# Performance work log

Measured on AMD Instinct MI355X. Metric: run time of the kernel, lower is better.

The kernel has to match this reference:

```python
import jax, jax.numpy as jnp
import numpy as np

HEADS = 4
DIM_HEAD = 32


def setup_inputs() -> dict:
    key = jax.random.key(0)
    k1, k2, k3, k4 = jax.random.split(key, 4)
    dim = 64
    hidden = HEADS * DIM_HEAD  # 128
    x = jax.random.normal(k1, (1, dim, 16, 16, 16), jnp.float32)
    # Conv3d 1x1 kernels collapse to [out_ch, in_ch] matrices
    w_qkv = jax.random.normal(k2, (hidden * 3, dim), jnp.float32) * 0.05
    w_out = jax.random.normal(k3, (dim, hidden), jnp.float32) * 0.05
    b_out = jax.random.normal(k4, (dim,), jnp.float32) * 0.05
    return {"x": x, "w_qkv": w_qkv, "w_out": w_out, "b_out": b_out}


def reference(x, w_qkv, w_out, b_out):
    scale = DIM_HEAD ** -0.5
    b, c, dz, dy, dx = x.shape
    n = dz * dy * dx
    xf = x.reshape(b, c, n)  # flatten spatial dims
    # 1x1 Conv3d (no bias) == channel matmul: [b, 3*hidden, n]
    qkv = jnp.einsum('oc,bcn->bon', w_qkv, xf)
    q, k, v = jnp.split(qkv, 3, axis=1)  # each [b, hidden, n]
    def split_heads(t):
        return t.reshape(b, HEADS, DIM_HEAD, n)  # [b, h, d, n]
    q, k, v = split_heads(q), split_heads(k), split_heads(v)
    q = q * scale
    # sim[b,h,i,j] = sum_d q[b,h,d,i] k[b,h,d,j]
    sim = jnp.einsum('bhdi,bhdj->bhij', q, k)
    sim = sim - jax.lax.stop_gradient(jnp.max(sim, axis=-1, keepdims=True))
    attn = jax.nn.softmax(sim, axis=-1)
    # out[b,h,i,d] = sum_j attn[b,h,i,j] v[b,h,d,j]
    out = jnp.einsum('bhij,bhdj->bhid', attn, v)
    # 'b h (z y x) d -> b (h d) z y x'
    out = out.transpose(0, 1, 3, 2).reshape(b, HEADS * DIM_HEAD, n)
    # final 1x1 Conv3d with bias
    y = jnp.einsum('oc,bcn->bon', w_out, out) + b_out[None, :, None]
    return y.reshape(b, -1, dz, dy, dx)
```

## Files before the change

kernel.cpp:

```cpp
#include <hip/hip_runtime.h>


typedef _Float16 f16x8 __attribute__((ext_vector_type(8)));
typedef _Float16 f16x4 __attribute__((ext_vector_type(4)));
typedef _Float16 f16x2v __attribute__((ext_vector_type(2)));
typedef __fp16 fp16x2n __attribute__((ext_vector_type(2)));
typedef float f32x4 __attribute__((ext_vector_type(4)));

static __device__ inline f16x4 pack4(float a, float b, float c, float d) {
  f16x4 r;
  r.x = (_Float16)a; r.y = (_Float16)b; r.z = (_Float16)c; r.w = (_Float16)d;
  return r;
}
static __device__ inline f16x4 pack4_rtz(float a, float b, float c, float d) {
  fp16x2n lo = __builtin_amdgcn_cvt_pkrtz(a, b);
  fp16x2n hi = __builtin_amdgcn_cvt_pkrtz(c, d);
  f16x4 r;
  r.x = (_Float16)lo.x; r.y = (_Float16)lo.y;
  r.z = (_Float16)hi.x; r.w = (_Float16)hi.y;
  return r;
}
static __device__ inline f16x2v pack2(float a, float b) {
  f16x2v r;
  r.x = (_Float16)a; r.y = (_Float16)b;
  return r;
}

__global__ __launch_bounds__(256) void qkv_kernel(
    const float* __restrict__ x, const float* __restrict__ w,
    _Float16* __restrict__ qo, _Float16* __restrict__ ko, _Float16* __restrict__ vo)
{
  __shared__ __align__(16) float xs[64 * 68];
  __shared__ __align__(16) float wsb[32 * 68];
  const int t = threadIdx.x;
  const int n0 = blockIdx.x * 64;
  const int o0 = blockIdx.y * 32;
  #pragma unroll
  for (int i = 0; i < 4; ++i) {
    int ch = t + i * 256;
    int c = ch >> 4, p = ch & 15;
    *reinterpret_cast<float4*>(&xs[c * 68 + p * 4]) =
        *reinterpret_cast<const float4*>(&x[c * 4096 + n0 + p * 4]);
  }
  #pragma unroll
  for (int i = 0; i < 2; ++i) {
    int ch = t + i * 256;
    int o = ch >> 4, p = ch & 15;
    *reinterpret_cast<float4*>(&wsb[o * 68 + p * 4]) =
        *reinterpret_cast<const float4*>(&w[(o0 + o) * 64 + p * 4]);
  }
  __syncthreads();
  const int oL = (t >> 5) * 4;
  const int nL = (t & 31) * 2;
  float acc[4][2] = {};
  for (int c4 = 0; c4 < 64; c4 += 4) {
    float2 xa[4];
    #pragma unroll
    for (int k = 0; k < 4; ++k)
      xa[k] = *reinterpret_cast<const float2*>(&xs[(c4 + k) * 68 + nL]);
    #pragma unroll
    for (int i = 0; i < 4; ++i) {
      float4 wv = *reinterpret_cast<const float4*>(&wsb[(oL + i) * 68 + c4]);
      acc[i][0] += wv.x * xa[0].x + wv.y * xa[1].x + wv.z * xa[2].x + wv.w * xa[3].x;
      acc[i][1] += wv.x * xa[0].y + wv.y * xa[1].y + wv.z * xa[2].y + wv.w * xa[3].y;
    }
  }
  const float qs = 0.17677669529663689f * 1.4426950408889634f;
  if (o0 < 128) {
    int ho = o0 >> 5;
    #pragma unroll
    for (int j = 0; j < 2; ++j) {
      int n = n0 + nL + j;
      *reinterpret_cast<f16x4*>(&qo[(ho * 4096 + n) * 32 + oL]) =
          pack4(acc[0][j] * qs, acc[1][j] * qs, acc[2][j] * qs, acc[3][j] * qs);
    }
  } else if (o0 < 256) {
    int ho = (o0 - 128) >> 5;
    #pragma unroll
    for (int j = 0; j < 2; ++j) {
      int n = n0 + nL + j;
      *reinterpret_cast<f16x4*>(&ko[(ho * 4096 + n) * 32 + oL]) =
          pack4(acc[0][j], acc[1][j], acc[2][j], acc[3][j]);
    }
  } else {
    #pragma unroll
    for (int i = 0; i < 4; ++i) {
      *reinterpret_cast<f16x2v*>(&vo[(size_t)(o0 - 256 + oL + i) * 4096 + n0 + nL]) =
          pack2(acc[i][0], acc[i][1]);
    }
  }
}

__global__ __launch_bounds__(512, 4) void attn_kernel(
    const _Float16* __restrict__ qg, const _Float16* __restrict__ kg,
    const _Float16* __restrict__ vg, _Float16* __restrict__ Opart,
    float* __restrict__ lpart, int jlen)
{
  __shared__ __align__(16) _Float16 Ks[2][64 * 40];
  __shared__ __align__(16) _Float16 Vs[2][32 * 72];
  const int t = threadIdx.x;
  const int ck = blockIdx.x;
  const int qt = blockIdx.y;
  const int h  = blockIdx.z;
  const int w = t >> 6;
  const int lane = t & 63;
  const int m = lane & 15;
  const int quad = lane >> 4;
  const int qw = qt * 256 + w * 32;

  f16x8 aq[2];
  #pragma unroll
  for (int g = 0; g < 2; ++g)
    aq[g] = *reinterpret_cast<const f16x8*>(
        &qg[(h * 4096 + qw + g * 16 + m) * 32 + quad * 8]);

  f32x4 acc[2][2];
  #pragma unroll
  for (int g = 0; g < 2; ++g) {
    acc[g][0] = f32x4{0.f, 0.f, 0.f, 0.f};
    acc[g][1] = f32x4{0.f, 0.f, 0.f, 0.f};
  }
  float ls[2] = {0.f, 0.f};

  const int jbeg = ck * jlen;
  const bool isK = (t < 256);
  const _Float16* gp;
  int ldsoff;
  if (isK) {
    int kr = t >> 2, ksg = t & 3;
    gp = kg + (size_t)(h * 4096 + jbeg + kr) * 32 + ksg * 8;
    ldsoff = kr * 40 + ksg * 8;
  } else {
    int c = t - 256, vr = c >> 3, vsg = c & 7;
    gp = vg + (size_t)(h * 32 + vr) * 4096 + jbeg + vsg * 8;
    ldsoff = vr * 72 + vsg * 8;
  }

  if (isK)
    *reinterpret_cast<uint4*>(&Ks[0][ldsoff]) = *reinterpret_cast<const uint4*>(gp);
  else
    *reinterpret_cast<uint4*>(&Vs[0][ldsoff]) = *reinterpret_cast<const uint4*>(gp);
  __syncthreads();

  for (int it = 0; it < jlen; it += 64) {
    const int buf = (it >> 6) & 1;
    if (it + 64 < jlen) {
      if (isK)
        *reinterpret_cast<uint4*>(&Ks[buf ^ 1][ldsoff]) =
            *reinterpret_cast<const uint4*>(gp + (size_t)(it + 64) * 32);
      else
        *reinterpret_cast<uint4*>(&Vs[buf ^ 1][ldsoff]) =
            *reinterpret_cast<const uint4*>(gp + (it + 64));
    }
    #pragma unroll
    for (int jt = 0; jt < 4; ++jt) {
      f16x8 kf = *reinterpret_cast<const f16x8*>(&Ks[buf][(jt * 16 + m) * 40 + quad * 8]);
      f16x4 vf0 = *reinterpret_cast<const f16x4*>(&Vs[buf][m * 72 + jt * 16 + quad * 4]);
      f16x4 vf1 = *reinterpret_cast<const f16x4*>(&Vs[buf][(16 + m) * 72 + jt * 16 + quad * 4]);
      f32x4 z = {0.f, 0.f, 0.f, 0.f};
      f32x4 sT[2];
      #pragma unroll
      for (int g = 0; g < 2; ++g)
        sT[g] = __builtin_amdgcn_mfma_f32_16x16x32_f16(kf, aq[g], z, 0, 0, 0);
      #pragma unroll
      for (int g = 0; g < 2; ++g) {
        float p0 = exp2f(sT[g][0]), p1 = exp2f(sT[g][1]);
        float p2 = exp2f(sT[g][2]), p3 = exp2f(sT[g][3]);
        ls[g] += (p0 + p1) + (p2 + p3);
        f16x4 p = pack4_rtz(p0, p1, p2, p3);
        acc[g][0] = __builtin_amdgcn_mfma_f32_16x16x16f16(p, vf0, acc[g][0], 0, 0, 0);
        acc[g][1] = __builtin_amdgcn_mfma_f32_16x16x16f16(p, vf1, acc[g][1], 0, 0, 0);
      }
    }
    __syncthreads();
  }

  #pragma unroll
  for (int g = 0; g < 2; ++g) {
    ls[g] += __shfl_xor(ls[g], 16);
    ls[g] += __shfl_xor(ls[g], 32);
  }
  const size_t cb = (size_t)(ck * 4 + h) * 4096;
  #pragma unroll
  for (int g = 0; g < 2; ++g) {
    #pragma unroll
    for (int dt = 0; dt < 2; ++dt) {
      #pragma unroll
      for (int r = 0; r < 4; ++r) {
        int q = qw + g * 16 + quad * 4 + r;
        Opart[(cb + q) * 32 + dt * 16 + m] = (_Float16)acc[g][dt][r];
      }
    }
  }
  if (quad == 0) {
    #pragma unroll
    for (int g = 0; g < 2; ++g)
      lpart[cb + qw + g * 16 + m] = ls[g];
  }
}

__global__ __launch_bounds__(512) void out_kernel(
    const _Float16* __restrict__ Opart, const float* __restrict__ lpart,
    const float* __restrict__ wo, const float* __restrict__ bo,
    float* __restrict__ y)
{
  __shared__ __align__(16) float as[16 * 132];
  __shared__ __align__(16) float wsh[64 * 132];
  __shared__ float linv[64];
  const int t = threadIdx.x;
  const int nb = blockIdx.x * 16;
  if (t < 64) {
    int h = t >> 4, r = t & 15;
    float s = 0.f;
    #pragma unroll
    for (int ck = 0; ck < 8; ++ck)
      s += lpart[(size_t)(ck * 4 + h) * 4096 + nb + r];
    linv[t] = 1.f / s;
  }
  {
    int ch = t;
    #pragma unroll
    for (int i = 0; i < 4; ++i, ch += 512) {
      int r = ch >> 5, p = ch & 31;
      *reinterpret_cast<float4*>(&wsh[r * 132 + p * 4]) =
          *reinterpret_cast<const float4*>(&wo[r * 128 + p * 4]);
    }
  }
  __syncthreads();
  {
    int r = t >> 5, p = t & 31;
    int h = p >> 3, d4 = (p & 7) * 4;
    float sx = 0.f, sy = 0.f, sz = 0.f, sw = 0.f;
    #pragma unroll
    for (int ck = 0; ck < 8; ++ck) {
      f16x4 o4 = *reinterpret_cast<const f16x4*>(
          &Opart[((size_t)(ck * 4 + h) * 4096 + nb + r) * 32 + d4]);
      sx += (float)o4.x; sy += (float)o4.y; sz += (float)o4.z; sw += (float)o4.w;
    }
    float inv = linv[h * 16 + r];
    float4 s = {sx * inv, sy * inv, sz * inv, sw * inv};
    *reinterpret_cast<float4*>(&as[r * 132 + p * 4]) = s;
  }
  __syncthreads();
  const int oL = (t >> 4) * 2;
  const int n = t & 15;
  float acc[2] = {0.f, 0.f};
  for (int c = 0; c < 128; c += 4) {
    float4 a = *reinterpret_cast<const float4*>(&as[n * 132 + c]);
    #pragma unroll
    for (int i = 0; i < 2; ++i) {
      float4 wv = *reinterpret_cast<const float4*>(&wsh[(oL + i) * 132 + c]);
      acc[i] += wv.x * a.x + wv.y * a.y + wv.z * a.z + wv.w * a.w;
    }
  }
  #pragma unroll
  for (int i = 0; i < 2; ++i) {
    y[(size_t)(oL + i) * 4096 + nb + n] = acc[i] + bo[oL + i];
  }
}

extern "C" void kernel_launch(void* const* d_in, const int* in_sizes, int n_in,
                              void* d_out, int out_size, void* d_ws, size_t ws_size,
                              hipStream_t stream) {
  (void)in_sizes; (void)n_in; (void)out_size; (void)ws_size;
  const float* x     = (const float*)d_in[0];
  const float* w_qkv = (const float*)d_in[1];
  const float* w_out = (const float*)d_in[2];
  const float* b_out = (const float*)d_in[3];
  float* y = (float*)d_out;
  _Float16* qb = (_Float16*)d_ws;
  _Float16* kb = qb + 524288;
  _Float16* vb = kb + 524288;
  _Float16* Opart = vb + 524288;
  float* lpart = (float*)(Opart + 4194304);

  qkv_kernel<<<dim3(64, 12), 256, 0, stream>>>(x, w_qkv, qb, kb, vb);
  attn_kernel<<<dim3(8, 16, 4), 512, 0, stream>>>(qb, kb, vb, Opart, lpart, 4096 / 8);
  out_kernel<<<256, 512, 0, stream>>>(Opart, lpart, w_out, b_out, y);
}
```

Baseline: 98.27 us.

## Rebalance attention split: 256-thread blocks, 4 key chunks, 32 query tiles

Attention blocks shrink from 512 to 256 threads (4 waves, 128 queries per block), and the key dimension is split into 4 chunks instead of 8. Each thread now loads both a K and a V segment per stage instead of splitting threads between K and V. The grid keeps the same number of workgroups but each one handles a longer key range. This halves the partial outputs written and reduced by the output kernel, at the cost of longer serial loops per block and less parallelism across key chunks.

New measurement: 100.3 us. +2.0%, slower.

```diff
diff --git a/kernel.cpp b/kernel.cpp
--- a/kernel.cpp
+++ b/kernel.cpp
@@ -91,7 +91,7 @@
   }
 }
 
-__global__ __launch_bounds__(512, 4) void attn_kernel(
+__global__ __launch_bounds__(256, 4) void attn_kernel(
     const _Float16* __restrict__ qg, const _Float16* __restrict__ kg,
     const _Float16* __restrict__ vg, _Float16* __restrict__ Opart,
     float* __restrict__ lpart, int jlen)
@@ -106,7 +106,7 @@
   const int lane = t & 63;
   const int m = lane & 15;
   const int quad = lane >> 4;
-  const int qw = qt * 256 + w * 32;
+  const int qw = qt * 128 + w * 32;
 
   f16x8 aq[2];
   #pragma unroll
@@ -123,34 +123,24 @@
   float ls[2] = {0.f, 0.f};
 
   const int jbeg = ck * jlen;
-  const bool isK = (t < 256);
-  const _Float16* gp;
-  int ldsoff;
-  if (isK) {
-    int kr = t >> 2, ksg = t & 3;
-    gp = kg + (size_t)(h * 4096 + jbeg + kr) * 32 + ksg * 8;
-    ldsoff = kr * 40 + ksg * 8;
-  } else {
-    int c = t - 256, vr = c >> 3, vsg = c & 7;
-    gp = vg + (size_t)(h * 32 + vr) * 4096 + jbeg + vsg * 8;
-    ldsoff = vr * 72 + vsg * 8;
-  }
-
-  if (isK)
-    *reinterpret_cast<uint4*>(&Ks[0][ldsoff]) = *reinterpret_cast<const uint4*>(gp);
-  else
-    *reinterpret_cast<uint4*>(&Vs[0][ldsoff]) = *reinterpret_cast<const uint4*>(gp);
+  const int kr = t >> 2, ksg = t & 3;
+  const int vr = t >> 3, vsg = t & 7;
+  const _Float16* kgp = kg + (size_t)(h * 4096 + jbeg + kr) * 32 + ksg * 8;
+  const _Float16* vgp = vg + (size_t)(h * 32 + vr) * 4096 + jbeg + vsg * 8;
+
+  *reinterpret_cast<uint4*>(&Ks[0][kr * 40 + ksg * 8]) =
+      *reinterpret_cast<const uint4*>(kgp);
+  *reinterpret_cast<uint4*>(&Vs[0][vr * 72 + vsg * 8]) =
+      *reinterpret_cast<const uint4*>(vgp);
   __syncthreads();
 
   for (int it = 0; it < jlen; it += 64) {
     const int buf = (it >> 6) & 1;
     if (it + 64 < jlen) {
-      if (isK)
-        *reinterpret_cast<uint4*>(&Ks[buf ^ 1][ldsoff]) =
-            *reinterpret_cast<const uint4*>(gp + (size_t)(it + 64) * 32);
-      else
-        *reinterpret_cast<uint4*>(&Vs[buf ^ 1][ldsoff]) =
-            *reinterpret_cast<const uint4*>(gp + (it + 64));
+      *reinterpret_cast<uint4*>(&Ks[buf ^ 1][kr * 40 + ksg * 8]) =
+          *reinterpret_cast<const uint4*>(kgp + (size_t)(it + 64) * 32);
+      *reinterpret_cast<uint4*>(&Vs[buf ^ 1][vr * 72 + vsg * 8]) =
+          *reinterpret_cast<const uint4*>(vgp + it + 64);
     }
     #pragma unroll
     for (int jt = 0; jt < 4; ++jt) {
@@ -213,7 +203,7 @@
     int h = t >> 4, r = t & 15;
     float s = 0.f;
     #pragma unroll
-    for (int ck = 0; ck < 8; ++ck)
+    for (int ck = 0; ck < 4; ++ck)
       s += lpart[(size_t)(ck * 4 + h) * 4096 + nb + r];
     linv[t] = 1.f / s;
   }
@@ -232,7 +222,7 @@
     int h = p >> 3, d4 = (p & 7) * 4;
     float sx = 0.f, sy = 0.f, sz = 0.f, sw = 0.f;
     #pragma unroll
-    for (int ck = 0; ck < 8; ++ck) {
+    for (int ck = 0; ck < 4; ++ck) {
       f16x4 o4 = *reinterpret_cast<const f16x4*>(
           &Opart[((size_t)(ck * 4 + h) * 4096 + nb + r) * 32 + d4]);
       sx += (float)o4.x; sy += (float)o4.y; sz += (float)o4.z; sw += (float)o4.w;
@@ -272,9 +262,9 @@
   _Float16* kb = qb + 524288;
   _Float16* vb = kb + 524288;
   _Float16* Opart = vb + 524288;
-  float* lpart = (float*)(Opart + 4194304);
+  float* lpart = (float*)(Opart + 2097152);
 
   qkv_kernel<<<dim3(64, 12), 256, 0, stream>>>(x, w_qkv, qb, kb, vb);
-  attn_kernel<<<dim3(8, 16, 4), 512, 0, stream>>>(qb, kb, vb, Opart, lpart, 4096 / 8);
+  attn_kernel<<<dim3(4, 32, 4), 256, 0, stream>>>(qb, kb, vb, Opart, lpart, 4096 / 4);
   out_kernel<<<256, 512, 0, stream>>>(Opart, lpart, w_out, b_out, y);
 }
```

## Reduce split-K attention partials in last-arriving block via atomic counter

Applied to the files above, without the earlier changes.

Moves the combination of the 8 split-K partial outputs and softmax denominators out of out_kernel and into attn_kernel. An atomic counter per (query tile, head) lets the last finishing block sum and normalise the partials and write a single fp16 O tensor. out_kernel then reads only O, which cuts its global reads by about eightfold. The costs are a threadfence, an atomic and a tail reduction done serially by one block per tile, plus an extra memset launch to clear the counters.

Measured after the change: 242.7 us. 147% more time.

```diff
diff --git a/kernel.cpp b/kernel.cpp
--- a/kernel.cpp
+++ b/kernel.cpp
@@ -94,10 +94,12 @@
 __global__ __launch_bounds__(512, 4) void attn_kernel(
     const _Float16* __restrict__ qg, const _Float16* __restrict__ kg,
     const _Float16* __restrict__ vg, _Float16* __restrict__ Opart,
-    float* __restrict__ lpart, int jlen)
+    _Float16* __restrict__ O, float* __restrict__ lpart,
+    unsigned int* __restrict__ cnt, int jlen)
 {
   __shared__ __align__(16) _Float16 Ks[2][64 * 40];
   __shared__ __align__(16) _Float16 Vs[2][32 * 72];
+  __shared__ int isLast;
   const int t = threadIdx.x;
   const int ck = blockIdx.x;
   const int qt = blockIdx.y;
@@ -197,26 +199,55 @@
     for (int g = 0; g < 2; ++g)
       lpart[cb + qw + g * 16 + m] = ls[g];
   }
+
+  __threadfence();
+  if (t == 0) {
+    unsigned int old = atomicAdd(&cnt[qt * 4 + h], 1u);
+    isLast = (old == 7u);
+  }
+  __syncthreads();
+  if (isLast) {
+    __threadfence();
+    const int qL = t >> 1;
+    const int d0 = (t & 1) * 16;
+    const int q = qt * 256 + qL;
+    float lsum = 0.f;
+    #pragma unroll
+    for (int c2 = 0; c2 < 8; ++c2)
+      lsum += lpart[(size_t)(c2 * 4 + h) * 4096 + q];
+    const float inv = 1.f / lsum;
+    float s[16];
+    #pragma unroll
+    for (int i = 0; i < 16; ++i) s[i] = 0.f;
+    #pragma unroll
+    for (int c2 = 0; c2 < 8; ++c2) {
+      const _Float16* src = &Opart[((size_t)(c2 * 4 + h) * 4096 + q) * 32 + d0];
+      #pragma unroll
+      for (int b4 = 0; b4 < 4; ++b4) {
+        f16x4 v4 = *reinterpret_cast<const f16x4*>(src + b4 * 4);
+        s[b4 * 4 + 0] += (float)v4.x; s[b4 * 4 + 1] += (float)v4.y;
+        s[b4 * 4 + 2] += (float)v4.z; s[b4 * 4 + 3] += (float)v4.w;
+      }
+    }
+    _Float16* dst = &O[((size_t)h * 4096 + q) * 32 + d0];
+    f16x8 o8;
+    #pragma unroll
+    for (int i = 0; i < 8; ++i) o8[i] = (_Float16)(s[i] * inv);
+    *reinterpret_cast<f16x8*>(dst) = o8;
+    #pragma unroll
+    for (int i = 0; i < 8; ++i) o8[i] = (_Float16)(s[8 + i] * inv);
+    *reinterpret_cast<f16x8*>(dst + 8) = o8;
+  }
 }
 
 __global__ __launch_bounds__(512) void out_kernel(
-    const _Float16* __restrict__ Opart, const float* __restrict__ lpart,
-    const float* __restrict__ wo, const float* __restrict__ bo,
-    float* __restrict__ y)
+    const _Float16* __restrict__ O, const float* __restrict__ wo,
+    const float* __restrict__ bo, float* __restrict__ y)
 {
   __shared__ __align__(16) float as[16 * 132];
   __shared__ __align__(16) float wsh[64 * 132];
-  __shared__ float linv[64];
   const int t = threadIdx.x;
   const int nb = blockIdx.x * 16;
-  if (t < 64) {
-    int h = t >> 4, r = t & 15;
-    float s = 0.f;
-    #pragma unroll
-    for (int ck = 0; ck < 8; ++ck)
-      s += lpart[(size_t)(ck * 4 + h) * 4096 + nb + r];
-    linv[t] = 1.f / s;
-  }
   {
     int ch = t;
     #pragma unroll
@@ -226,19 +257,12 @@
           *reinterpret_cast<const float4*>(&wo[r * 128 + p * 4]);
     }
   }
-  __syncthreads();
   {
     int r = t >> 5, p = t & 31;
     int h = p >> 3, d4 = (p & 7) * 4;
-    float sx = 0.f, sy = 0.f, sz = 0.f, sw = 0.f;
-    #pragma unroll
-    for (int ck = 0; ck < 8; ++ck) {
-      f16x4 o4 = *reinterpret_cast<const f16x4*>(
-          &Opart[((size_t)(ck * 4 + h) * 4096 + nb + r) * 32 + d4]);
-      sx += (float)o4.x; sy += (float)o4.y; sz += (float)o4.z; sw += (float)o4.w;
-    }
-    float inv = linv[h * 16 + r];
-    float4 s = {sx * inv, sy * inv, sz * inv, sw * inv};
+    f16x4 o4 = *reinterpret_cast<const f16x4*>(
+        &O[((size_t)h * 4096 + nb + r) * 32 + d4]);
+    float4 s = {(float)o4.x, (float)o4.y, (float)o4.z, (float)o4.w};
     *reinterpret_cast<float4*>(&as[r * 132 + p * 4]) = s;
   }
   __syncthreads();
@@ -272,9 +296,12 @@
   _Float16* kb = qb + 524288;
   _Float16* vb = kb + 524288;
   _Float16* Opart = vb + 524288;
-  float* lpart = (float*)(Opart + 4194304);
-
+  _Float16* O     = Opart + 4194304;
+  float* lpart = (float*)(O + 524288);
+  unsigned int* cnt = (unsigned int*)(lpart + 131072);
+
+  hipMemsetAsync(cnt, 0, 64 * sizeof(unsigned int), stream);
   qkv_kernel<<<dim3(64, 12), 256, 0, stream>>>(x, w_qkv, qb, kb, vb);
-  attn_kernel<<<dim3(8, 16, 4), 512, 0, stream>>>(qb, kb, vb, Opart, lpart, 4096 / 8);
-  out_kernel<<<256, 512, 0, stream>>>(Opart, lpart, w_out, b_out, y);
-}
+  attn_kernel<<<dim3(8, 16, 4), 512, 0, stream>>>(qb, kb, vb, Opart, O, lpart, cnt, 4096 / 8);
+  out_kernel<<<256, 512, 0, stream>>>(O, w_out, b_out, y);
+}
```
